# Kernel tuning notes

Hardware: AMD Instinct MI355X
Metric: run time of the kernel (lower is better)

Reference implementation:

```python
import jax, jax.numpy as jnp
import numpy as np


def setup_inputs() -> dict:
    key = jax.random.key(0)
    k1, k2 = jax.random.split(key)
    z = jax.random.normal(k1, (16, 2048, 512), dtype=jnp.float32)
    embedding = jax.random.normal(k2, (8192, 512), dtype=jnp.float32)
    return {"z": z, "embedding": embedding}


def reference(z, embedding):
    BETA = 0.25
    B, N, D = z.shape
    n_codes = embedding.shape[0]
    flat_z = z.reshape(-1, D)  # [M, D], M = B*N
    # squared euclidean distances: ||z||^2 - 2 z.e^T + ||e||^2 -> [M, n_codes]
    dist = (jnp.sum(flat_z * flat_z, axis=1, keepdims=True)
            - 2.0 * jnp.matmul(flat_z, embedding.T)
            + jnp.sum(embedding * embedding, axis=1))
    codes = jnp.argmin(dist, axis=1)  # [M]
    z_q = embedding[codes].reshape(B, N, D)
    # straight-through estimator
    z_q_st = z + jax.lax.stop_gradient(z_q - z)
    loss = BETA * jnp.mean((z_q_st - jax.lax.stop_gradient(z)) ** 2)
    # codebook usage stats (equivalent to one_hot.mean(0))
    counts = jnp.zeros((n_codes,), dtype=flat_z.dtype).at[codes].add(1.0)
    avg_probs = counts / flat_z.shape[0]
    perp = jnp.exp(-jnp.sum(avg_probs * jnp.log(avg_probs + 1e-10)))
    return z_q_st, codes.reshape(B, N), loss, perp
```

## Files before the change

### kernel.cpp

```cpp
#include <hip/hip_runtime.h>
#include <stdint.h>
#include <stddef.h>

#define M_ROWS 32768
#define N_CODES 8192
#define K_DIM 512
#define BM 128
#define BN 128
#define BK 64
#define KITERS (K_DIM / BK)
#define CAND_CAP (3u*1024u*1024u)
#define LCAP 512u
#define TAU2 2.0f

#define OFF_CODES 16777216
#define OFF_LOSS  (16777216 + 32768)
#define OFF_PERP  (16777216 + 32768 + 1)

using short8  = __attribute__((ext_vector_type(8))) short;
using ushort8 = __attribute__((ext_vector_type(8))) unsigned short;
using f32x4   = __attribute__((ext_vector_type(4))) float;

typedef unsigned short u16;
typedef unsigned int   u32;
typedef unsigned long long u64;

__device__ __forceinline__ u32 ford(float f) {
    u32 u = __float_as_uint(f);
    return (u & 0x80000000u) ? ~u : (u | 0x80000000u);
}
__device__ __forceinline__ float fordinv(u32 u) {
    u32 v = (u & 0x80000000u) ? (u & 0x7FFFFFFFu) : ~u;
    return __uint_as_float(v);
}
__device__ __forceinline__ u16 f2bf(float f) {
    u32 u = __float_as_uint(f);
    u = u + 0x7FFFu + ((u >> 16) & 1u);
    return (u16)(u >> 16);
}

__device__ __forceinline__ void ldg_to_lds16(const u16* g, u16* l) {
    __builtin_amdgcn_global_load_lds((__attribute__((address_space(1))) void*)(g),
                                     (__attribute__((address_space(3))) void*)(l),
                                     16, 0, 0);
}

__global__ void k_convert(const float* __restrict__ src, u16* __restrict__ dst,
                          float* __restrict__ nrm2, int nrows,
                          u32* rowMin, u64* rowBest, u32* counts, u32* candCnt,
                          float* fsum, u32* ticket) {
    if (rowMin) {
        int g = blockIdx.x * blockDim.x + threadIdx.x;
        if (g < M_ROWS) { rowMin[g] = 0xFFFFFFFFu; rowBest[g] = ~0ull; }
        if (g < N_CODES) counts[g] = 0u;
        if (g == 0) { *candCnt = 0u; *fsum = 0.f; *ticket = 0u; }
    }
    int row  = blockIdx.x * 4 + (threadIdx.x >> 6);
    int lane = threadIdx.x & 63;
    if (row >= nrows) return;
    const float* p = src + (size_t)row * K_DIM + lane * 8;
    float4 a = *(const float4*)p;
    float4 b = *(const float4*)(p + 4);
    ushort8 v;
    v[0]=f2bf(a.x); v[1]=f2bf(a.y); v[2]=f2bf(a.z); v[3]=f2bf(a.w);
    v[4]=f2bf(b.x); v[5]=f2bf(b.y); v[6]=f2bf(b.z); v[7]=f2bf(b.w);
    *(ushort8*)(dst + (size_t)row * K_DIM + lane * 8) = v;
    float ss = a.x*a.x + a.y*a.y + a.z*a.z + a.w*a.w
             + b.x*b.x + b.y*b.y + b.z*b.z + b.w*b.w;
    #pragma unroll
    for (int s = 32; s; s >>= 1) ss += __shfl_xor(ss, s);
    if (lane == 0) nrm2[row] = ss;
}

__global__ __launch_bounds__(256, 4)
void k_gemm(const u16* __restrict__ zb, const u16* __restrict__ eb,
            const float* __restrict__ en2, u32* __restrict__ rowMin,
            u32* __restrict__ candCnt, u64* __restrict__ cand) {
    __shared__ __align__(16) u16 As[BM * BK];
    __shared__ __align__(16) u16 Bs[BN * BK];
    __shared__ float en2s[BN];
    __shared__ u32 threshL[BM];
    __shared__ u64 candBuf[LCAP];
    __shared__ u32 ldsCnt, ldsBase;

    const int tid  = threadIdx.x;
    const int lane = tid & 63;
    const int wave = tid >> 6;
    const int rowTile = blockIdx.x * BM;
    const int nTile   = blockIdx.y * BN;
    const int wm = (wave >> 1) * 64;
    const int wn = (wave & 1) * 64;

    if (tid < BN) { en2s[tid] = en2[nTile + tid]; threshL[tid] = 0xFFFFFFFFu; }
    if (tid == 0) ldsCnt = 0u;

    const int srow = (lane >> 3);
    const int sg   = (lane & 7) ^ ((lane >> 3) & 7);
    const u16* gA[4]; const u16* gB[4]; u16* lA[4]; u16* lB[4];
    #pragma unroll
    for (int t = 0; t < 4; t++) {
        int i = wave * 4 + t;
        gA[t] = zb + (size_t)(rowTile + i * 8 + srow) * K_DIM + sg * 8;
        gB[t] = eb + (size_t)(nTile   + i * 8 + srow) * K_DIM + sg * 8;
        lA[t] = As + i * 512;
        lB[t] = Bs + i * 512;
    }

    int aoff[4], boff[4];
    const int q = lane >> 4;
    #pragma unroll
    for (int t = 0; t < 4; t++) {
        int R  = wm + t * 16 + (lane & 15);
        aoff[t] = (R * 8 + (q ^ (R & 7))) * 16;
        int Rn = wn + t * 16 + (lane & 15);
        boff[t] = (Rn * 8 + (q ^ (Rn & 7))) * 16;
    }

    f32x4 acc[4][4] = {};

    for (int kk = 0; kk < KITERS; kk++) {
        const int ko = kk * BK;
        #pragma unroll
        for (int t = 0; t < 4; t++) {
            ldg_to_lds16(gA[t] + ko, lA[t]);
            ldg_to_lds16(gB[t] + ko, lB[t]);
        }
        __syncthreads();
        short8 af[4], bf_[4];
        #pragma unroll
        for (int t = 0; t < 4; t++) {
            af[t]  = *(const short8*)((const char*)As + aoff[t]);
            bf_[t] = *(const short8*)((const char*)Bs + boff[t]);
        }
        #pragma unroll
        for (int i = 0; i < 4; i++)
            #pragma unroll
            for (int j = 0; j < 4; j++)
                acc[i][j] = __builtin_amdgcn_mfma_f32_16x16x32_bf16(af[i], bf_[j], acc[i][j], 0, 0, 0);
        #pragma unroll
        for (int t = 0; t < 4; t++) {
            af[t]  = *(const short8*)((const char*)As + (aoff[t] ^ 64));
            bf_[t] = *(const short8*)((const char*)Bs + (boff[t] ^ 64));
        }
        #pragma unroll
        for (int i = 0; i < 4; i++)
            #pragma unroll
            for (int j = 0; j < 4; j++)
                acc[i][j] = __builtin_amdgcn_mfma_f32_16x16x32_bf16(af[i], bf_[j], acc[i][j], 0, 0, 0);
        __syncthreads();
    }

    float e2v[4];
    #pragma unroll
    for (int j = 0; j < 4; j++) e2v[j] = en2s[wn + j * 16 + (lane & 15)];
    #pragma unroll
    for (int i = 0; i < 4; i++)
        #pragma unroll
        for (int j = 0; j < 4; j++)
            #pragma unroll
            for (int r = 0; r < 4; r++)
                acc[i][j][r] = e2v[j] - 2.0f * acc[i][j][r];

    float rm[4][4];
    #pragma unroll
    for (int i = 0; i < 4; i++)
        #pragma unroll
        for (int r = 0; r < 4; r++)
            rm[i][r] = fminf(fminf(acc[i][0][r], acc[i][1][r]),
                             fminf(acc[i][2][r], acc[i][3][r]));
    #pragma unroll
    for (int d = 1; d < 16; d <<= 1)
        #pragma unroll
        for (int i = 0; i < 4; i++)
            #pragma unroll
            for (int r = 0; r < 4; r++)
                rm[i][r] = fminf(rm[i][r], __shfl_xor(rm[i][r], d));

    if ((lane & 15) == 0) {
        #pragma unroll
        for (int i = 0; i < 4; i++)
            #pragma unroll
            for (int r = 0; r < 4; r++) {
                int lrow = wm + i * 16 + (lane >> 4) * 4 + r;
                u32 o = ford(rm[i][r]);
                atomicMin(&threshL[lrow], o);
                u32 old = atomicMin(&rowMin[rowTile + lrow], o);
                atomicMin(&threshL[lrow], old);
            }
    }
    __syncthreads();

    #pragma unroll
    for (int i = 0; i < 4; i++) {
        #pragma unroll
        for (int r = 0; r < 4; r++) {
            int lrow = wm + i * 16 + (lane >> 4) * 4 + r;
            float th = fordinv(threshL[lrow]) + TAU2;
            #pragma unroll
            for (int j = 0; j < 4; j++) {
                float sv = acc[i][j][r];
                if (sv <= th) {
                    u32 code = (u32)(nTile + wn + j * 16 + (lane & 15));
                    u64 pk = ((u64)ford(sv) << 32) |
                             (u64)(((u32)(rowTile + lrow) << 13) | code);
                    u32 idx = atomicAdd(&ldsCnt, 1u);
                    if (idx < LCAP) candBuf[idx] = pk;
                    else { u32 g = atomicAdd(candCnt, 1u);
                           if (g < CAND_CAP) cand[g] = pk; }
                }
            }
        }
    }
    __syncthreads();
    if (tid == 0) {
        u32 n = ldsCnt < LCAP ? ldsCnt : LCAP;
        ldsBase = atomicAdd(candCnt, n);
    }
    __syncthreads();
    u32 n = ldsCnt < LCAP ? ldsCnt : LCAP;
    for (u32 k2 = tid; k2 < n; k2 += 256) {
        u32 g = ldsBase + k2;
        if (g < CAND_CAP) cand[g] = candBuf[k2];
    }
}

__global__ void k_refine(const float* __restrict__ z, const float* __restrict__ emb,
                         const float* __restrict__ en2, const u32* __restrict__ candCnt,
                         const u64* __restrict__ cand, const u32* __restrict__ rowMin,
                         u64* __restrict__ rowBest) {
    u32 cnt = *candCnt; if (cnt > CAND_CAP) cnt = CAND_CAP;
    int gt = blockIdx.x * blockDim.x + threadIdx.x;
    u32 wid = (u32)(gt >> 6);
    int lane = gt & 63;
    u32 nw = (u32)((gridDim.x * blockDim.x) >> 6);
    for (u32 base = wid * 64u; base < cnt; base += nw * 64u) {
        u32 ci = base + (u32)lane;
        u32 row = 0, code = 0;
        bool live = false;
        if (ci < cnt) {
            u64 pk = cand[ci];
            u32 rc = (u32)pk;
            row = rc >> 13; code = rc & (N_CODES - 1);
            float ad = fordinv((u32)(pk >> 32));
            float gm = fordinv(rowMin[row]);
            live = (ad <= gm + TAU2);
        }
        u64 mask = __ballot(live);
        while (mask) {
            int s = (int)(__ffsll((long long)mask) - 1);
            mask &= mask - 1;
            u32 srow  = __shfl(row,  s);
            u32 scode = __shfl(code, s);
            const float4* zp = (const float4*)(z + (size_t)srow * K_DIM) + lane * 2;
            const float4* ep = (const float4*)(emb + (size_t)scode * K_DIM) + lane * 2;
            float4 a0 = zp[0], a1 = zp[1], b0 = ep[0], b1 = ep[1];
            float d = a0.x*b0.x + a0.y*b0.y + a0.z*b0.z + a0.w*b0.w
                    + a1.x*b1.x + a1.y*b1.y + a1.z*b1.z + a1.w*b1.w;
            #pragma unroll
            for (int sh = 32; sh; sh >>= 1) d += __shfl_xor(d, sh);
            if (lane == 0) {
                float sv = en2[scode] - 2.0f * d;
                u64 bk = ((u64)ford(sv) << 32) | (u64)scode;
                atomicMin(rowBest + srow, bk);
            }
        }
    }
}

__global__ void k_output(const u64* __restrict__ rowBest, const float* __restrict__ emb,
                         float* __restrict__ out, u32* __restrict__ counts) {
    int row = blockIdx.x * 4 + (threadIdx.x >> 7);
    int t   = threadIdx.x & 127;
    u64 pk = rowBest[row];
    u32 code = (u32)(pk & 0xFFFFFFFFull);
    float4 v = ((const float4*)(emb + (size_t)code * K_DIM))[t];
    ((float4*)(out + (size_t)row * K_DIM))[t] = v;
    if (t == 0) {
        out[OFF_CODES + row] = (float)code;
        atomicAdd(&counts[code], 1u);
    }
}

__global__ void k_final(const u64* __restrict__ rowBest, const float* __restrict__ zn2,
                        const u32* __restrict__ counts, float* __restrict__ out,
                        float* __restrict__ fsum, u32* __restrict__ ticket) {
    __shared__ float red[256];
    __shared__ int lastBlk;
    __shared__ float lossSumSh;
    int t = threadIdx.x;
    float s1 = 0.f;
    for (int r = blockIdx.x * 256 + t; r < M_ROWS; r += gridDim.x * 256)
        s1 += zn2[r] + fordinv((u32)(rowBest[r] >> 32));
    red[t] = s1; __syncthreads();
    for (int w = 128; w; w >>= 1) { if (t < w) red[t] += red[t + w]; __syncthreads(); }
    if (t == 0) {
        atomicAdd(fsum, red[0]);
        __threadfence();
        lastBlk = (atomicAdd(ticket, 1u) == gridDim.x - 1) ? 1 : 0;
    }
    __syncthreads();
    if (!lastBlk) return;
    if (t == 0) lossSumSh = atomicAdd(fsum, 0.0f);
    float s2 = 0.f;
    for (int c = t; c < N_CODES; c += 256) {
        float p = (float)counts[c] * (1.0f / (float)M_ROWS);
        s2 += p * logf(p + 1e-10f);
    }
    red[t] = s2; __syncthreads();
    for (int w = 128; w; w >>= 1) { if (t < w) red[t] += red[t + w]; __syncthreads(); }
    if (t == 0) {
        out[OFF_LOSS] = 0.25f * lossSumSh / ((float)M_ROWS * (float)K_DIM);
        out[OFF_PERP] = expf(-red[0]);
    }
}

#define WS_ZB      ((size_t)0)
#define WS_EB      ((size_t)33554432)
#define WS_EN2     ((size_t)41943040)
#define WS_ZN2     ((size_t)41975808)
#define WS_ROWMIN  ((size_t)42106880)
#define WS_ROWBEST ((size_t)42237952)
#define WS_COUNTS  ((size_t)42500096)
#define WS_CANDCNT ((size_t)42532864)
#define WS_CAND    ((size_t)42533120)

extern "C" void kernel_launch(void* const* d_in, const int* in_sizes, int n_in,
                              void* d_out, int out_size, void* d_ws, size_t ws_size,
                              hipStream_t stream) {
    const float* z   = (const float*)d_in[0];
    const float* emb = (const float*)d_in[1];
    float* out = (float*)d_out;
    char* ws = (char*)d_ws;

    u16*  zb      = (u16*)(ws + WS_ZB);
    u16*  eb      = (u16*)(ws + WS_EB);
    float* en2    = (float*)(ws + WS_EN2);
    float* zn2    = (float*)(ws + WS_ZN2);
    u32*  rowMin  = (u32*)(ws + WS_ROWMIN);
    u64*  rowBest = (u64*)(ws + WS_ROWBEST);
    u32*  counts  = (u32*)(ws + WS_COUNTS);
    u32*  candCnt = (u32*)(ws + WS_CANDCNT);
    float* fsum   = (float*)(ws + WS_CANDCNT + 8);
    u32*  ticket  = (u32*)(ws + WS_CANDCNT + 12);
    u64*  cand    = (u64*)(ws + WS_CAND);

    k_convert<<<dim3(M_ROWS / 4), dim3(256), 0, stream>>>(z, zb, zn2, M_ROWS,
                                                          rowMin, rowBest, counts, candCnt, fsum, ticket);
    k_convert<<<dim3(N_CODES / 4), dim3(256), 0, stream>>>(emb, eb, en2, N_CODES,
                                                           nullptr, nullptr, nullptr, nullptr, nullptr, nullptr);
    k_gemm<<<dim3(M_ROWS / BM, N_CODES / BN), dim3(256), 0, stream>>>(zb, eb, en2, rowMin, candCnt, cand);
    k_refine<<<dim3(1024), dim3(256), 0, stream>>>(z, emb, en2, candCnt, cand, rowMin, rowBest);
    k_output<<<dim3(M_ROWS / 4), dim3(512), 0, stream>>>(rowBest, emb, out, counts);
    k_final<<<dim3(32), dim3(256), 0, stream>>>(rowBest, zn2, counts, out, fsum, ticket);
}
```

Before: 627.8 us.

## Merge conversion launches and fuse refine/output/final into one cooperative kernel

The two bf16 conversion launches become a single launch that picks z or the embedding by block index. The refine, gather-output and loss/perplexity kernels are fused into one cooperative kernel separated by grid.sync. The output phase now accumulates the loss while it gathers rows, and the ticket-based last-block logic is dropped. This removes several launch gaps and a separate pass over rowBest, at the cost of grid-wide barriers and a cooperative launch limited to 1024 blocks.

```diff
diff --git a/kernel.cpp b/kernel.cpp
--- a/kernel.cpp
+++ b/kernel.cpp
@@ -1,6 +1,9 @@
 #include <hip/hip_runtime.h>
+#include <hip/hip_cooperative_groups.h>
 #include <stdint.h>
 #include <stddef.h>
+
+namespace cg = cooperative_groups;
 
 #define M_ROWS 32768
 #define N_CODES 8192
@@ -45,28 +48,32 @@
                                      16, 0, 0);
 }
 
-__global__ void k_convert(const float* __restrict__ src, u16* __restrict__ dst,
-                          float* __restrict__ nrm2, int nrows,
+__global__ void k_convert(const float* __restrict__ z, const float* __restrict__ emb,
+                          u16* __restrict__ zb, u16* __restrict__ eb,
+                          float* __restrict__ zn2, float* __restrict__ en2,
                           u32* rowMin, u64* rowBest, u32* counts, u32* candCnt,
-                          float* fsum, u32* ticket) {
-    if (rowMin) {
-        int g = blockIdx.x * blockDim.x + threadIdx.x;
+                          float* fsum) {
+    int b = blockIdx.x;
+    const float* src; u16* dst; float* nrm2; int row;
+    if (b < 8192) {
+        int g = b * blockDim.x + threadIdx.x;
         if (g < M_ROWS) { rowMin[g] = 0xFFFFFFFFu; rowBest[g] = ~0ull; }
         if (g < N_CODES) counts[g] = 0u;
-        if (g == 0) { *candCnt = 0u; *fsum = 0.f; *ticket = 0u; }
-    }
-    int row  = blockIdx.x * 4 + (threadIdx.x >> 6);
+        if (g == 0) { *candCnt = 0u; *fsum = 0.f; }
+        src = z; dst = zb; nrm2 = zn2; row = b * 4 + (threadIdx.x >> 6);
+    } else {
+        src = emb; dst = eb; nrm2 = en2; row = (b - 8192) * 4 + (threadIdx.x >> 6);
+    }
     int lane = threadIdx.x & 63;
-    if (row >= nrows) return;
     const float* p = src + (size_t)row * K_DIM + lane * 8;
     float4 a = *(const float4*)p;
-    float4 b = *(const float4*)(p + 4);
+    float4 bb = *(const float4*)(p + 4);
     ushort8 v;
     v[0]=f2bf(a.x); v[1]=f2bf(a.y); v[2]=f2bf(a.z); v[3]=f2bf(a.w);
-    v[4]=f2bf(b.x); v[5]=f2bf(b.y); v[6]=f2bf(b.z); v[7]=f2bf(b.w);
+    v[4]=f2bf(bb.x); v[5]=f2bf(bb.y); v[6]=f2bf(bb.z); v[7]=f2bf(bb.w);
     *(ushort8*)(dst + (size_t)row * K_DIM + lane * 8) = v;
     float ss = a.x*a.x + a.y*a.y + a.z*a.z + a.w*a.w
-             + b.x*b.x + b.y*b.y + b.z*b.z + b.w*b.w;
+             + bb.x*bb.x + bb.y*bb.y + bb.z*bb.z + bb.w*bb.w;
     #pragma unroll
     for (int s = 32; s; s >>= 1) ss += __shfl_xor(ss, s);
     if (lane == 0) nrm2[row] = ss;
@@ -224,93 +231,97 @@
     }
 }
 
-__global__ void k_refine(const float* __restrict__ z, const float* __restrict__ emb,
-                         const float* __restrict__ en2, const u32* __restrict__ candCnt,
-                         const u64* __restrict__ cand, const u32* __restrict__ rowMin,
-                         u64* __restrict__ rowBest) {
-    u32 cnt = *candCnt; if (cnt > CAND_CAP) cnt = CAND_CAP;
-    int gt = blockIdx.x * blockDim.x + threadIdx.x;
-    u32 wid = (u32)(gt >> 6);
-    int lane = gt & 63;
-    u32 nw = (u32)((gridDim.x * blockDim.x) >> 6);
-    for (u32 base = wid * 64u; base < cnt; base += nw * 64u) {
-        u32 ci = base + (u32)lane;
-        u32 row = 0, code = 0;
-        bool live = false;
-        if (ci < cnt) {
-            u64 pk = cand[ci];
-            u32 rc = (u32)pk;
-            row = rc >> 13; code = rc & (N_CODES - 1);
-            float ad = fordinv((u32)(pk >> 32));
-            float gm = fordinv(rowMin[row]);
-            live = (ad <= gm + TAU2);
-        }
-        u64 mask = __ballot(live);
-        while (mask) {
-            int s = (int)(__ffsll((long long)mask) - 1);
-            mask &= mask - 1;
-            u32 srow  = __shfl(row,  s);
-            u32 scode = __shfl(code, s);
-            const float4* zp = (const float4*)(z + (size_t)srow * K_DIM) + lane * 2;
-            const float4* ep = (const float4*)(emb + (size_t)scode * K_DIM) + lane * 2;
-            float4 a0 = zp[0], a1 = zp[1], b0 = ep[0], b1 = ep[1];
-            float d = a0.x*b0.x + a0.y*b0.y + a0.z*b0.z + a0.w*b0.w
-                    + a1.x*b1.x + a1.y*b1.y + a1.z*b1.z + a1.w*b1.w;
-            #pragma unroll
-            for (int sh = 32; sh; sh >>= 1) d += __shfl_xor(d, sh);
-            if (lane == 0) {
-                float sv = en2[scode] - 2.0f * d;
-                u64 bk = ((u64)ford(sv) << 32) | (u64)scode;
-                atomicMin(rowBest + srow, bk);
-            }
-        }
-    }
-}
-
-__global__ void k_output(const u64* __restrict__ rowBest, const float* __restrict__ emb,
-                         float* __restrict__ out, u32* __restrict__ counts) {
-    int row = blockIdx.x * 4 + (threadIdx.x >> 7);
-    int t   = threadIdx.x & 127;
-    u64 pk = rowBest[row];
-    u32 code = (u32)(pk & 0xFFFFFFFFull);
-    float4 v = ((const float4*)(emb + (size_t)code * K_DIM))[t];
-    ((float4*)(out + (size_t)row * K_DIM))[t] = v;
-    if (t == 0) {
-        out[OFF_CODES + row] = (float)code;
-        atomicAdd(&counts[code], 1u);
-    }
-}
-
-__global__ void k_final(const u64* __restrict__ rowBest, const float* __restrict__ zn2,
-                        const u32* __restrict__ counts, float* __restrict__ out,
-                        float* __restrict__ fsum, u32* __restrict__ ticket) {
+__global__ __launch_bounds__(256, 4)
+void k_tail(const float* __restrict__ z, const float* __restrict__ emb,
+            const float* __restrict__ en2, const float* __restrict__ zn2,
+            const u32* __restrict__ candCnt, const u64* __restrict__ cand,
+            const u32* __restrict__ rowMin, u64* __restrict__ rowBest,
+            u32* __restrict__ counts, float* __restrict__ out,
+            float* __restrict__ fsum) {
+    cg::grid_group grid = cg::this_grid();
     __shared__ float red[256];
-    __shared__ int lastBlk;
-    __shared__ float lossSumSh;
-    int t = threadIdx.x;
-    float s1 = 0.f;
-    for (int r = blockIdx.x * 256 + t; r < M_ROWS; r += gridDim.x * 256)
-        s1 += zn2[r] + fordinv((u32)(rowBest[r] >> 32));
-    red[t] = s1; __syncthreads();
-    for (int w = 128; w; w >>= 1) { if (t < w) red[t] += red[t + w]; __syncthreads(); }
-    if (t == 0) {
-        atomicAdd(fsum, red[0]);
-        __threadfence();
-        lastBlk = (atomicAdd(ticket, 1u) == gridDim.x - 1) ? 1 : 0;
-    }
-    __syncthreads();
-    if (!lastBlk) return;
-    if (t == 0) lossSumSh = atomicAdd(fsum, 0.0f);
-    float s2 = 0.f;
-    for (int c = t; c < N_CODES; c += 256) {
-        float p = (float)counts[c] * (1.0f / (float)M_ROWS);
-        s2 += p * logf(p + 1e-10f);
-    }
-    red[t] = s2; __syncthreads();
-    for (int w = 128; w; w >>= 1) { if (t < w) red[t] += red[t + w]; __syncthreads(); }
-    if (t == 0) {
-        out[OFF_LOSS] = 0.25f * lossSumSh / ((float)M_ROWS * (float)K_DIM);
-        out[OFF_PERP] = expf(-red[0]);
+
+    {
+        u32 cnt = *candCnt; if (cnt > CAND_CAP) cnt = CAND_CAP;
+        int gt = blockIdx.x * 256 + threadIdx.x;
+        u32 wid = (u32)(gt >> 6);
+        int lane = gt & 63;
+        u32 nw = (u32)((gridDim.x * 256) >> 6);
+        for (u32 base = wid * 64u; base < cnt; base += nw * 64u) {
+            u32 ci = base + (u32)lane;
+            u32 row = 0, code = 0;
+            bool live = false;
+            if (ci < cnt) {
+                u64 pk = cand[ci];
+                u32 rc = (u32)pk;
+                row = rc >> 13; code = rc & (N_CODES - 1);
+                float ad = fordinv((u32)(pk >> 32));
+                float gm = fordinv(rowMin[row]);
+                live = (ad <= gm + TAU2);
+            }
+            u64 mask = __ballot(live);
+            while (mask) {
+                int s = (int)(__ffsll((long long)mask) - 1);
+                mask &= mask - 1;
+                u32 srow  = __shfl(row,  s);
+                u32 scode = __shfl(code, s);
+                const float4* zp = (const float4*)(z + (size_t)srow * K_DIM) + lane * 2;
+                const float4* ep = (const float4*)(emb + (size_t)scode * K_DIM) + lane * 2;
+                float4 a0 = zp[0], a1 = zp[1], b0 = ep[0], b1 = ep[1];
+                float d = a0.x*b0.x + a0.y*b0.y + a0.z*b0.z + a0.w*b0.w
+                        + a1.x*b1.x + a1.y*b1.y + a1.z*b1.z + a1.w*b1.w;
+                #pragma unroll
+                for (int sh = 32; sh; sh >>= 1) d += __shfl_xor(d, sh);
+                if (lane == 0) {
+                    float sv = en2[scode] - 2.0f * d;
+                    u64 bk = ((u64)ford(sv) << 32) | (u64)scode;
+                    atomicMin(rowBest + srow, bk);
+                }
+            }
+        }
+    }
+    grid.sync();
+
+    {
+        float s1 = 0.f;
+        int rl = threadIdx.x >> 7;
+        int t  = threadIdx.x & 127;
+        #pragma unroll 4
+        for (int it = 0; it < 16; it++) {
+            int row = blockIdx.x * 32 + it * 2 + rl;
+            u64 pk = rowBest[row];
+            u32 code = (u32)(pk & 0xFFFFFFFFull);
+            float4 v = ((const float4*)(emb + (size_t)code * K_DIM))[t];
+            ((float4*)(out + (size_t)row * K_DIM))[t] = v;
+            if (t == 0) {
+                out[OFF_CODES + row] = (float)code;
+                atomicAdd(&counts[code], 1u);
+                s1 += zn2[row] + fordinv((u32)(pk >> 32));
+            }
+        }
+        red[threadIdx.x] = s1; __syncthreads();
+        for (int w = 128; w; w >>= 1) {
+            if (threadIdx.x < w) red[threadIdx.x] += red[threadIdx.x + w];
+            __syncthreads();
+        }
+        if (threadIdx.x == 0) atomicAdd(fsum, red[0]);
+    }
+    grid.sync();
+
+    if (blockIdx.x == 0) {
+        int t = threadIdx.x;
+        float s2 = 0.f;
+        for (int c = t; c < N_CODES; c += 256) {
+            float p = (float)atomicAdd(&counts[c], 0u) * (1.0f / (float)M_ROWS);
+            s2 += p * logf(p + 1e-10f);
+        }
+        red[t] = s2; __syncthreads();
+        for (int w = 128; w; w >>= 1) { if (t < w) red[t] += red[t + w]; __syncthreads(); }
+        if (t == 0) {
+            float lossSum = atomicAdd(fsum, 0.0f);
+            out[OFF_LOSS] = 0.25f * lossSum / ((float)M_ROWS * (float)K_DIM);
+            out[OFF_PERP] = expf(-red[0]);
+        }
     }
 }
 
@@ -341,15 +352,13 @@
     u32*  counts  = (u32*)(ws + WS_COUNTS);
     u32*  candCnt = (u32*)(ws + WS_CANDCNT);
     float* fsum   = (float*)(ws + WS_CANDCNT + 8);
-    u32*  ticket  = (u32*)(ws + WS_CANDCNT + 12);
     u64*  cand    = (u64*)(ws + WS_CAND);
 
-    k_convert<<<dim3(M_ROWS / 4), dim3(256), 0, stream>>>(z, zb, zn2, M_ROWS,
-                                                          rowMin, rowBest, counts, candCnt, fsum, ticket);
-    k_convert<<<dim3(N_CODES / 4), dim3(256), 0, stream>>>(emb, eb, en2, N_CODES,
-                                                           nullptr, nullptr, nullptr, nullptr, nullptr, nullptr);
+    k_convert<<<dim3(8192 + 2048), dim3(256), 0, stream>>>(z, emb, zb, eb, zn2, en2,
+                                                           rowMin, rowBest, counts, candCnt, fsum);
     k_gemm<<<dim3(M_ROWS / BM, N_CODES / BN), dim3(256), 0, stream>>>(zb, eb, en2, rowMin, candCnt, cand);
-    k_refine<<<dim3(1024), dim3(256), 0, stream>>>(z, emb, en2, candCnt, cand, rowMin, rowBest);
-    k_output<<<dim3(M_ROWS / 4), dim3(512), 0, stream>>>(rowBest, emb, out, counts);
-    k_final<<<dim3(32), dim3(256), 0, stream>>>(rowBest, zn2, counts, out, fsum, ticket);
-}
+    void* args[] = { (void*)&z, (void*)&emb, (void*)&en2, (void*)&zn2,
+                     (void*)&candCnt, (void*)&cand, (void*)&rowMin, (void*)&rowBest,
+                     (void*)&counts, (void*)&out, (void*)&fsum };
+    hipLaunchCooperativeKernel((const void*)k_tail, dim3(1024), dim3(256), args, 0, stream);
+}
```

New measurement: 826.7 us. 31.7% more time.
